# Kernel tuning notes

Measured on AMD Instinct MI355X. Metric: run time of the kernel, lower is better.

## Reference

```python
import jax, jax.numpy as jnp
import numpy as np

# dims: batch, query/key grid HxW, channels, heads (== W for the final matmul to be consistent)
B, H, W, DIM, HEADS = 4, 64, 64, 512, 64
QKV = DIM // HEADS          # per-head projection width (8)
SCALE = QKV ** -0.5         # self.qkv_dim ** -0.5


def setup_inputs() -> dict:
    key = jax.random.key(0)
    k1, k2, k3, k4 = jax.random.split(key, 4)
    x = jax.random.normal(k1, (B, H, W, DIM), dtype=jnp.float32)
    # AttnVector weights, init std=0.01 as in nn.init.normal_(self.w, std=0.01)
    w_q = jax.random.normal(k2, (DIM, HEADS, QKV), dtype=jnp.float32) * 0.01
    w_k = jax.random.normal(k3, (DIM, HEADS, QKV), dtype=jnp.float32) * 0.01
    w_v = jax.random.normal(k4, (DIM, HEADS, QKV), dtype=jnp.float32) * 0.01
    return {"x": x, "w_q": w_q, "w_k": w_k, "w_v": w_v}


def reference(x, w_q, w_k, w_v):
    # q, k, v projections: einsum 'bhwc,cnp->bhwnp' -> [B,H,W,HEADS,QKV]
    q = jnp.einsum('bhwc,cnp->bhwnp', x, w_q)
    k = jnp.einsum('bhwc,cnp->bhwnp', x, w_k)
    v = jnp.einsum('bhwc,cnp->bhwnp', x, w_v)
    # Literal math of torch.einsum('bhwc,bpqd->bhwpq', q, k): the contracted
    # labels c and d appear only once each, so each tensor is summed over its
    # feature axes independently and the result is an outer product over
    # spatial positions: weights[b,h,w,p,q] = sum(q[b,h,w]) * sum(k[b,p,q]).
    qs = q.sum(axis=(-2, -1))  # [B,H,W]
    ks = k.sum(axis=(-2, -1))  # [B,H,W]
    weights = qs[:, :, :, None, None] * ks[:, None, None, :, :]  # [B,H,W,H,W]
    # dropout (p=0.1) is identity in eval mode; scale applied BEFORE softmax,
    # exactly as in the source (weights *= scale; softmax(dim=-1)).
    weights = jax.nn.softmax(weights * SCALE, axis=-1)
    # weights @ value: batch dims (B,H,W), matmul (H_p, W_q) @ (heads==W_q, QKV)
    attn = jnp.einsum('bhwpq,bhwqd->bhwpd', weights, v)  # [B,H,W,H,QKV]
    return attn
```

## Files before the change

kernel.cpp:

```cpp
#include <hip/hip_runtime.h>
#include <hip/hip_bf16.h>
#include <math.h>


#define SCALE 0.35355339059327373f
#define LOG2E 1.4426950408889634f

typedef __attribute__((ext_vector_type(8))) _Float16 f16x8;
typedef __attribute__((ext_vector_type(4))) _Float16 f16x4;
typedef __attribute__((ext_vector_type(4))) float f32x4;

__device__ __forceinline__ void gl16(const void* g, void* l) {
    __builtin_amdgcn_global_load_lds(
        (const __attribute__((address_space(1))) unsigned int*)g,
        (__attribute__((address_space(3))) unsigned int*)l, 16, 0, 0);
}

__global__ __launch_bounds__(256) void k_prep(const float* __restrict__ wq,
                                              const float* __restrict__ wk,
                                              const float* __restrict__ wv,
                                              float* __restrict__ wqs,
                                              float* __restrict__ wks,
                                              _Float16* __restrict__ whf) {
    __shared__ float tile[64][65];
    if (blockIdx.x >= 64) {
        int gw = ((int)blockIdx.x - 64) * 4 + (threadIdx.x >> 6);
        int lane = threadIdx.x & 63;
        const float* src = (gw < 512) ? wq : wk;
        int c = gw & 511;
        const float4* row = (const float4*)(src + (size_t)c * 512);
        float4 a = row[lane * 2], b = row[lane * 2 + 1];
        float s = a.x + a.y + a.z + a.w + b.x + b.y + b.z + b.w;
#pragma unroll
        for (int off = 32; off; off >>= 1) s += __shfl_xor(s, off);
        if (lane == 0) {
            if (gw < 512) wqs[c] = s; else wks[c] = s;
        }
        return;
    }
    const int ti = (int)blockIdx.x >> 3;
    const int tj = (int)blockIdx.x & 7;
    const int r = threadIdx.x >> 4;
    const int c4 = (threadIdx.x & 15) * 4;
#pragma unroll
    for (int i = 0; i < 4; ++i) {
        int kl = r + i * 16;
        float4 v = *(const float4*)(wv + (size_t)(ti * 64 + kl) * 512 + tj * 64 + c4);
        tile[kl][c4 + 0] = v.x; tile[kl][c4 + 1] = v.y;
        tile[kl][c4 + 2] = v.z; tile[kl][c4 + 3] = v.w;
    }
    __syncthreads();
#pragma unroll
    for (int i = 0; i < 4; ++i) {
        int nl = r + i * 16;
        int n = tj * 64 + nl;
        f16x4 h4;
        h4[0] = (_Float16)tile[c4 + 0][nl];
        h4[1] = (_Float16)tile[c4 + 1][nl];
        h4[2] = (_Float16)tile[c4 + 2][nl];
        h4[3] = (_Float16)tile[c4 + 3][nl];
        *(f16x4*)(whf + (size_t)n * 512 + ti * 64 + c4) = h4;
    }
}

__global__ __launch_bounds__(256) void k_qsks(const float* __restrict__ x,
                                              const float* __restrict__ wqs,
                                              const float* __restrict__ wks,
                                              float* __restrict__ qs,
                                              float* __restrict__ ks,
                                              _Float16* __restrict__ xh) {
    int row = (int)blockIdx.x * 4 + (threadIdx.x >> 6);
    int lane = threadIdx.x & 63;
    const float4* xr = (const float4*)(x + (size_t)row * 512);
    const float4* q4 = (const float4*)wqs;
    const float4* k4 = (const float4*)wks;
    float4 xv0 = xr[lane * 2], xv1 = xr[lane * 2 + 1];
    float4 qv0 = q4[lane * 2], qv1 = q4[lane * 2 + 1];
    float4 kv0 = k4[lane * 2], kv1 = k4[lane * 2 + 1];
    float sq = xv0.x * qv0.x + xv0.y * qv0.y + xv0.z * qv0.z + xv0.w * qv0.w
             + xv1.x * qv1.x + xv1.y * qv1.y + xv1.z * qv1.z + xv1.w * qv1.w;
    float sk = xv0.x * kv0.x + xv0.y * kv0.y + xv0.z * kv0.z + xv0.w * kv0.w
             + xv1.x * kv1.x + xv1.y * kv1.y + xv1.z * kv1.z + xv1.w * kv1.w;
    f16x8 hv;
    hv[0] = (_Float16)xv0.x; hv[1] = (_Float16)xv0.y;
    hv[2] = (_Float16)xv0.z; hv[3] = (_Float16)xv0.w;
    hv[4] = (_Float16)xv1.x; hv[5] = (_Float16)xv1.y;
    hv[6] = (_Float16)xv1.z; hv[7] = (_Float16)xv1.w;
    *(f16x8*)(xh + (size_t)row * 512 + lane * 8) = hv;
#pragma unroll
    for (int off = 32; off; off >>= 1) {
        sq += __shfl_xor(sq, off);
        sk += __shfl_xor(sk, off);
    }
    if (lane == 0) { qs[row] = sq; ks[row] = sk; }
}

__global__ __launch_bounds__(64) void k_prep2(const float* __restrict__ ks,
                                              float* __restrict__ kmax,
                                              float* __restrict__ kmin,
                                              float* __restrict__ L) {
    int bp = blockIdx.x;
    int b = bp >> 6, p = bp & 63;
    int q = threadIdx.x;
    float v = ks[bp * 64 + q];
    float hi = v, lo = v;
#pragma unroll
    for (int off = 32; off; off >>= 1) {
        hi = fmaxf(hi, __shfl_xor(hi, off));
        lo = fminf(lo, __shfl_xor(lo, off));
    }
    if (q == 0) { kmax[bp] = hi; kmin[bp] = lo; }
    L[((b * 64 + q) * 16 + (p & 15)) * 4 + (p >> 4)] = v;
}

__global__ __launch_bounds__(256, 3) void k_vgemm(const _Float16* __restrict__ xh,
                                                  const _Float16* __restrict__ whf,
                                                  float* __restrict__ V) {
    __shared__ _Float16 As[128 * 64];
    __shared__ _Float16 Bs[128 * 64];

    const int tid = threadIdx.x;
    const int wave = tid >> 6, lane = tid & 63;
    const int mblk = (int)(blockIdx.x >> 2) * 128;
    const int nblk = (int)(blockIdx.x & 3) * 128;
    const int wm = wave >> 1, wn = wave & 1;
    const int arow = lane & 15, kgrp = lane >> 4;
    const int s7 = arow & 7;

    const _Float16* pa[4]; const _Float16* pb[4];
    _Float16* la[4]; _Float16* lb[4];
#pragma unroll
    for (int i = 0; i < 4; ++i) {
        const int g = i * 256 + tid;
        const int row = g >> 3, gp = g & 7;
        const int gs = (gp ^ (row & 7)) * 8;
        pa[i] = xh + (size_t)(mblk + row) * 512 + gs;
        pb[i] = whf + (size_t)(nblk + row) * 512 + gs;
        la[i] = As + g * 8;
        lb[i] = Bs + g * 8;
    }

    f32x4 acc[4][4];
#pragma unroll
    for (int mt = 0; mt < 4; ++mt)
#pragma unroll
        for (int nt = 0; nt < 4; ++nt) acc[mt][nt] = (f32x4){0.f, 0.f, 0.f, 0.f};

    for (int step = 0; step < 8; ++step) {
#pragma unroll
        for (int i = 0; i < 4; ++i) gl16(pa[i], la[i]);
#pragma unroll
        for (int i = 0; i < 4; ++i) gl16(pb[i], lb[i]);
#pragma unroll
        for (int i = 0; i < 4; ++i) { pa[i] += 64; pb[i] += 64; }
        __syncthreads();

#pragma unroll
        for (int sub = 0; sub < 2; ++sub) {
            f16x8 a[4], b[4];
            const int pg = ((sub * 4 + kgrp) ^ s7) * 8;
#pragma unroll
            for (int mt = 0; mt < 4; ++mt)
                a[mt] = *(const f16x8*)(As + (wm * 64 + mt * 16 + arow) * 64 + pg);
#pragma unroll
            for (int nt = 0; nt < 4; ++nt)
                b[nt] = *(const f16x8*)(Bs + (wn * 64 + nt * 16 + arow) * 64 + pg);
#pragma unroll
            for (int mt = 0; mt < 4; ++mt)
#pragma unroll
                for (int nt = 0; nt < 4; ++nt)
                    acc[mt][nt] = __builtin_amdgcn_mfma_f32_16x16x32_f16(a[mt], b[nt], acc[mt][nt], 0, 0, 0);
        }
        __syncthreads();
    }

    const int rbase = (lane >> 4) * 4;
#pragma unroll
    for (int mt = 0; mt < 4; ++mt)
#pragma unroll
        for (int nt = 0; nt < 4; ++nt) {
            const int col = nblk + wn * 64 + nt * 16 + arow;
#pragma unroll
            for (int r = 0; r < 4; ++r) {
                const int row = mblk + wm * 64 + mt * 16 + rbase + r;
                V[(size_t)row * 512 + col] = acc[mt][nt][r];
            }
        }
}

__global__ __launch_bounds__(256) void k_attn(float* __restrict__ io,
                                              const float* __restrict__ qs,
                                              const float* __restrict__ L,
                                              const float* __restrict__ kmax,
                                              const float* __restrict__ kmin) {
    __shared__ float vsm[16 * 520];
    __shared__ float Lsm[4096];
    const int tid = threadIdx.x;
    const int r0 = (int)blockIdx.x * 16;
    const int b = r0 >> 12;

    {
        const float4* vg = (const float4*)(io + (size_t)r0 * 512);
#pragma unroll
        for (int i = 0; i < 8; ++i) {
            int idx4 = tid + 256 * i;
            *(float4*)(vsm + (idx4 >> 7) * 520 + (idx4 & 127) * 4) = vg[idx4];
        }
        const float4* Lg = (const float4*)(L + (size_t)b * 4096);
#pragma unroll
        for (int i = 0; i < 4; ++i)
            *(float4*)(Lsm + (tid + 256 * i) * 4) = Lg[tid + 256 * i];
    }
    __syncthreads();

    const int m = tid >> 4, p0 = tid & 15;
    const float t2 = qs[r0 + m] * (SCALE * LOG2E);
    float rm2[4], den[4], acc[4][8];
#pragma unroll
    for (int j = 0; j < 4; ++j) {
        float khi = kmax[b * 64 + p0 + 16 * j];
        float klo = kmin[b * 64 + p0 + 16 * j];
        rm2[j] = (t2 >= 0.f) ? t2 * khi : t2 * klo;
        den[j] = 0.f;
#pragma unroll
        for (int d = 0; d < 8; ++d) acc[j][d] = 0.f;
    }
    const float* vrow = vsm + m * 520;
#pragma unroll 4
    for (int q = 0; q < 64; ++q) {
        const float4 kv = *(const float4*)(Lsm + (q * 16 + p0) * 4);
        const f32x4 v0 = *(const f32x4*)(vrow + q * 8);
        const f32x4 v1 = *(const f32x4*)(vrow + q * 8 + 4);
        const float kvj[4] = {kv.x, kv.y, kv.z, kv.w};
#pragma unroll
        for (int j = 0; j < 4; ++j) {
            const float e = exp2f(fmaf(t2, kvj[j], -rm2[j]));
            den[j] += e;
            acc[j][0] = fmaf(e, v0[0], acc[j][0]);
            acc[j][1] = fmaf(e, v0[1], acc[j][1]);
            acc[j][2] = fmaf(e, v0[2], acc[j][2]);
            acc[j][3] = fmaf(e, v0[3], acc[j][3]);
            acc[j][4] = fmaf(e, v1[0], acc[j][4]);
            acc[j][5] = fmaf(e, v1[1], acc[j][5]);
            acc[j][6] = fmaf(e, v1[2], acc[j][6]);
            acc[j][7] = fmaf(e, v1[3], acc[j][7]);
        }
    }
#pragma unroll
    for (int j = 0; j < 4; ++j) {
        const float inv = 1.0f / den[j];
        float4* o = (float4*)(io + (size_t)(r0 + m) * 512 + (p0 + 16 * j) * 8);
        o[0] = make_float4(acc[j][0] * inv, acc[j][1] * inv, acc[j][2] * inv, acc[j][3] * inv);
        o[1] = make_float4(acc[j][4] * inv, acc[j][5] * inv, acc[j][6] * inv, acc[j][7] * inv);
    }
}

extern "C" void kernel_launch(void* const* d_in, const int* in_sizes, int n_in,
                              void* d_out, int out_size, void* d_ws, size_t ws_size,
                              hipStream_t stream) {
    const float* x  = (const float*)d_in[0];
    const float* wq = (const float*)d_in[1];
    const float* wk = (const float*)d_in[2];
    const float* wv = (const float*)d_in[3];
    float* out = (float*)d_out;

    float* ws   = (float*)d_ws;
    float* qs   = ws;
    float* ks   = ws + 16384;
    float* wqs  = ws + 32768;
    float* wks  = ws + 33280;
    float* kmax = ws + 33792;
    float* kmin = ws + 34048;
    float* L    = ws + 34304;
    _Float16* whf = (_Float16*)(ws + 50688);
    _Float16* xh  = (_Float16*)(ws + 181760);

    hipLaunchKernelGGL(k_prep,  dim3(320),  dim3(256), 0, stream, wq, wk, wv, wqs, wks, whf);
    hipLaunchKernelGGL(k_qsks,  dim3(4096), dim3(256), 0, stream, x, wqs, wks, qs, ks, xh);
    hipLaunchKernelGGL(k_prep2, dim3(256),  dim3(64),  0, stream, ks, kmax, kmin, L);
    hipLaunchKernelGGL(k_vgemm, dim3(512),  dim3(256), 0, stream, xh, whf, out);
    hipLaunchKernelGGL(k_attn,  dim3(1024), dim3(256), 0, stream, out, qs, L, kmax, kmin);
}
```

Before: 140.0 us.

## Move softmax-weighted V accumulation onto MFMA with fp16 V and ones-column denominator

The attention kernel now computes exp weights per lane in fp16 and feeds them with a transposed fp16 V tile to 16x16x32 MFMA instructions. The denominator comes from a column of ones appended to V. The V GEMM now writes fp16 to a separate workspace instead of fp32 into the output buffer, and the L relayout in prep2 is dropped. This targets the scalar FMA and exp bottleneck and halves V traffic. The cost is fp16 rounding of both V and the softmax weights, and only 9 of 16 A rows of each MFMA carry useful data.

```diff
diff --git a/kernel.cpp b/kernel.cpp
--- a/kernel.cpp
+++ b/kernel.cpp
@@ -97,10 +97,8 @@
 
 __global__ __launch_bounds__(64) void k_prep2(const float* __restrict__ ks,
                                               float* __restrict__ kmax,
-                                              float* __restrict__ kmin,
-                                              float* __restrict__ L) {
+                                              float* __restrict__ kmin) {
     int bp = blockIdx.x;
-    int b = bp >> 6, p = bp & 63;
     int q = threadIdx.x;
     float v = ks[bp * 64 + q];
     float hi = v, lo = v;
@@ -110,12 +108,11 @@
         lo = fminf(lo, __shfl_xor(lo, off));
     }
     if (q == 0) { kmax[bp] = hi; kmin[bp] = lo; }
-    L[((b * 64 + q) * 16 + (p & 15)) * 4 + (p >> 4)] = v;
 }
 
 __global__ __launch_bounds__(256, 3) void k_vgemm(const _Float16* __restrict__ xh,
                                                   const _Float16* __restrict__ whf,
-                                                  float* __restrict__ V) {
+                                                  _Float16* __restrict__ vh) {
     __shared__ _Float16 As[128 * 64];
     __shared__ _Float16 Bs[128 * 64];
 
@@ -183,75 +180,100 @@
 #pragma unroll
             for (int r = 0; r < 4; ++r) {
                 const int row = mblk + wm * 64 + mt * 16 + rbase + r;
-                V[(size_t)row * 512 + col] = acc[mt][nt][r];
+                vh[(size_t)row * 512 + col] = (_Float16)acc[mt][nt][r];
             }
         }
 }
 
-__global__ __launch_bounds__(256) void k_attn(float* __restrict__ io,
-                                              const float* __restrict__ qs,
-                                              const float* __restrict__ L,
-                                              const float* __restrict__ kmax,
-                                              const float* __restrict__ kmin) {
-    __shared__ float vsm[16 * 520];
-    __shared__ float Lsm[4096];
+__global__ __launch_bounds__(256, 3) void k_attn2(const _Float16* __restrict__ vh,
+                                                  const float* __restrict__ qs,
+                                                  const float* __restrict__ ks,
+                                                  const float* __restrict__ kmax,
+                                                  const float* __restrict__ kmin,
+                                                  float* __restrict__ out) {
+    __shared__ _Float16 Vt[32 * 576];
     const int tid = threadIdx.x;
-    const int r0 = (int)blockIdx.x * 16;
+    const int r0 = (int)blockIdx.x * 32;
     const int b = r0 >> 12;
+    const int lane = tid & 63, wid = tid >> 6;
+    const int n = lane & 15, kgrp = lane >> 4;
 
     {
-        const float4* vg = (const float4*)(io + (size_t)r0 * 512);
-#pragma unroll
-        for (int i = 0; i < 8; ++i) {
-            int idx4 = tid + 256 * i;
-            *(float4*)(vsm + (idx4 >> 7) * 520 + (idx4 & 127) * 4) = vg[idx4];
+        const int r = tid >> 3, g = tid & 7;
+        f16x8 ones;
+#pragma unroll
+        for (int i = 0; i < 8; ++i) ones[i] = (_Float16)1.0f;
+        *(f16x8*)(Vt + r * 576 + 512 + g * 8) = ones;
+    }
+#pragma unroll
+    for (int c = 0; c < 8; ++c) {
+        const int ch = c * 256 + tid;
+        const int rr = ch >> 6, q = ch & 63;
+        f16x8 v = *(const f16x8*)(vh + (size_t)(r0 + rr) * 512 + q * 8);
+        const int gq = q >> 3, qi = q & 7;
+        _Float16* base = Vt + rr * 576 + qi;
+#pragma unroll
+        for (int d = 0; d < 8; ++d)
+            base[d * 64 + ((gq ^ d) * 8)] = v[d];
+    }
+
+    float4 kk[4][2][2];
+#pragma unroll
+    for (int nt = 0; nt < 4; ++nt)
+#pragma unroll
+        for (int ksi = 0; ksi < 2; ++ksi)
+#pragma unroll
+            for (int h = 0; h < 2; ++h)
+                kk[nt][ksi][h] = *(const float4*)(ks + b * 4096 + (nt * 16 + n) * 64
+                                                  + ksi * 32 + kgrp * 8 + h * 4);
+    float km[4], kn[4];
+#pragma unroll
+    for (int nt = 0; nt < 4; ++nt) {
+        km[nt] = kmax[b * 64 + nt * 16 + n];
+        kn[nt] = kmin[b * 64 + nt * 16 + n];
+    }
+    __syncthreads();
+
+    const int m = n;
+    const bool aval = (m <= 8);
+    const int abase0 = m * 64 + ((kgrp ^ (m & 7)) * 8);
+    const int abase1 = m * 64 + (((4 + kgrp) ^ (m & 7)) * 8);
+    const f16x8 azero = {};
+
+    for (int it = 0; it < 8; ++it) {
+        const int lp = wid * 8 + it;
+        const int r = r0 + lp;
+        const float t2 = qs[r] * (SCALE * LOG2E);
+        const f16x8 a0 = aval ? *(const f16x8*)(Vt + lp * 576 + abase0) : azero;
+        const f16x8 a1 = aval ? *(const f16x8*)(Vt + lp * 576 + abase1) : azero;
+
+#pragma unroll
+        for (int nt = 0; nt < 4; ++nt) {
+            const float rm2 = (t2 >= 0.f) ? t2 * km[nt] : t2 * kn[nt];
+            f16x8 b0, b1;
+#pragma unroll
+            for (int h = 0; h < 2; ++h) {
+                const float4 k0 = kk[nt][0][h];
+                const float4 k1 = kk[nt][1][h];
+                b0[h * 4 + 0] = (_Float16)exp2f(fmaf(t2, k0.x, -rm2));
+                b0[h * 4 + 1] = (_Float16)exp2f(fmaf(t2, k0.y, -rm2));
+                b0[h * 4 + 2] = (_Float16)exp2f(fmaf(t2, k0.z, -rm2));
+                b0[h * 4 + 3] = (_Float16)exp2f(fmaf(t2, k0.w, -rm2));
+                b1[h * 4 + 0] = (_Float16)exp2f(fmaf(t2, k1.x, -rm2));
+                b1[h * 4 + 1] = (_Float16)exp2f(fmaf(t2, k1.y, -rm2));
+                b1[h * 4 + 2] = (_Float16)exp2f(fmaf(t2, k1.z, -rm2));
+                b1[h * 4 + 3] = (_Float16)exp2f(fmaf(t2, k1.w, -rm2));
+            }
+            f32x4 acc = (f32x4){0.f, 0.f, 0.f, 0.f};
+            acc = __builtin_amdgcn_mfma_f32_16x16x32_f16(a0, b0, acc, 0, 0, 0);
+            acc = __builtin_amdgcn_mfma_f32_16x16x32_f16(a1, b1, acc, 0, 0, 0);
+            const float den = __shfl(acc[0], 32 + n);
+            const float inv = __builtin_amdgcn_rcpf(den);
+            if (lane < 32) {
+                float4 o = make_float4(acc[0] * inv, acc[1] * inv, acc[2] * inv, acc[3] * inv);
+                *(float4*)(out + (size_t)r * 512 + (nt * 16 + n) * 8 + kgrp * 4) = o;
+            }
         }
-        const float4* Lg = (const float4*)(L + (size_t)b * 4096);
-#pragma unroll
-        for (int i = 0; i < 4; ++i)
-            *(float4*)(Lsm + (tid + 256 * i) * 4) = Lg[tid + 256 * i];
-    }
-    __syncthreads();
-
-    const int m = tid >> 4, p0 = tid & 15;
-    const float t2 = qs[r0 + m] * (SCALE * LOG2E);
-    float rm2[4], den[4], acc[4][8];
-#pragma unroll
-    for (int j = 0; j < 4; ++j) {
-        float khi = kmax[b * 64 + p0 + 16 * j];
-        float klo = kmin[b * 64 + p0 + 16 * j];
-        rm2[j] = (t2 >= 0.f) ? t2 * khi : t2 * klo;
-        den[j] = 0.f;
-#pragma unroll
-        for (int d = 0; d < 8; ++d) acc[j][d] = 0.f;
-    }
-    const float* vrow = vsm + m * 520;
-#pragma unroll 4
-    for (int q = 0; q < 64; ++q) {
-        const float4 kv = *(const float4*)(Lsm + (q * 16 + p0) * 4);
-        const f32x4 v0 = *(const f32x4*)(vrow + q * 8);
-        const f32x4 v1 = *(const f32x4*)(vrow + q * 8 + 4);
-        const float kvj[4] = {kv.x, kv.y, kv.z, kv.w};
-#pragma unroll
-        for (int j = 0; j < 4; ++j) {
-            const float e = exp2f(fmaf(t2, kvj[j], -rm2[j]));
-            den[j] += e;
-            acc[j][0] = fmaf(e, v0[0], acc[j][0]);
-            acc[j][1] = fmaf(e, v0[1], acc[j][1]);
-            acc[j][2] = fmaf(e, v0[2], acc[j][2]);
-            acc[j][3] = fmaf(e, v0[3], acc[j][3]);
-            acc[j][4] = fmaf(e, v1[0], acc[j][4]);
-            acc[j][5] = fmaf(e, v1[1], acc[j][5]);
-            acc[j][6] = fmaf(e, v1[2], acc[j][6]);
-            acc[j][7] = fmaf(e, v1[3], acc[j][7]);
-        }
-    }
-#pragma unroll
-    for (int j = 0; j < 4; ++j) {
-        const float inv = 1.0f / den[j];
-        float4* o = (float4*)(io + (size_t)(r0 + m) * 512 + (p0 + 16 * j) * 8);
-        o[0] = make_float4(acc[j][0] * inv, acc[j][1] * inv, acc[j][2] * inv, acc[j][3] * inv);
-        o[1] = make_float4(acc[j][4] * inv, acc[j][5] * inv, acc[j][6] * inv, acc[j][7] * inv);
     }
 }
 
@@ -271,13 +293,13 @@
     float* wks  = ws + 33280;
     float* kmax = ws + 33792;
     float* kmin = ws + 34048;
-    float* L    = ws + 34304;
     _Float16* whf = (_Float16*)(ws + 50688);
     _Float16* xh  = (_Float16*)(ws + 181760);
+    _Float16* vh  = (_Float16*)(ws + 4376064);
 
     hipLaunchKernelGGL(k_prep,  dim3(320),  dim3(256), 0, stream, wq, wk, wv, wqs, wks, whf);
     hipLaunchKernelGGL(k_qsks,  dim3(4096), dim3(256), 0, stream, x, wqs, wks, qs, ks, xh);
-    hipLaunchKernelGGL(k_prep2, dim3(256),  dim3(64),  0, stream, ks, kmax, kmin, L);
-    hipLaunchKernelGGL(k_vgemm, dim3(512),  dim3(256), 0, stream, xh, whf, out);
-    hipLaunchKernelGGL(k_attn,  dim3(1024), dim3(256), 0, stream, out, qs, L, kmax, kmin);
-}
+    hipLaunchKernelGGL(k_prep2, dim3(256),  dim3(64),  0, stream, ks, kmax, kmin);
+    hipLaunchKernelGGL(k_vgemm, dim3(512),  dim3(256), 0, stream, xh, whf, vh);
+    hipLaunchKernelGGL(k_attn2, dim3(512),  dim3(256), 0, stream, vh, qs, ks, kmax, kmin, out);
+}
```

Measured after the change: 132.4 us. 1.06x faster.
